# Kernel tuning notes

Measured on AMD Instinct MI355X. Metric: run time of the kernel, lower is better.

## Reference

```python
import jax, jax.numpy as jnp
import numpy as np

N, TI, ENC_DIM, DEC_DIM, ATT_DIM = 32, 2000, 512, 512, 512


def setup_inputs() -> dict:
    key = jax.random.key(0)
    ks = jax.random.split(key, 8)
    enc_pad = jax.random.normal(ks[0], (N, TI, ENC_DIM), dtype=jnp.float32)
    dec_prev = jax.random.normal(ks[1], (N, DEC_DIM), dtype=jnp.float32)
    ali_prev = jax.random.uniform(ks[2], (N, TI), dtype=jnp.float32)
    # lengths in [Ti//2, Ti], force one full-length row (module uses max(enc_len) as mask width)
    enc_len = jax.random.randint(ks[3], (N,), TI // 2, TI + 1)
    enc_len = enc_len.at[0].set(TI)
    # learned params (nn.Linear layout: W [out, in])
    s_e = 1.0 / np.sqrt(ENC_DIM)
    s_d = 1.0 / np.sqrt(DEC_DIM)
    s_a = 1.0 / np.sqrt(ATT_DIM)
    W_enc = jax.random.uniform(ks[4], (ATT_DIM, ENC_DIM), minval=-s_e, maxval=s_e, dtype=jnp.float32)
    b_enc = jax.random.uniform(ks[5], (ATT_DIM,), minval=-s_e, maxval=s_e, dtype=jnp.float32)
    W_dec = jax.random.uniform(ks[6], (ATT_DIM, DEC_DIM), minval=-s_d, maxval=s_d, dtype=jnp.float32)
    w_v = jax.random.uniform(ks[7], (ATT_DIM,), minval=-s_a, maxval=s_a, dtype=jnp.float32)
    return {"enc_pad": enc_pad, "enc_len": enc_len, "dec_prev": dec_prev,
            "ali_prev": ali_prev, "W_enc": W_enc, "b_enc": b_enc,
            "W_dec": W_dec, "w_v": w_v}


def reference(enc_pad, enc_len, dec_prev, ali_prev, W_enc, b_enc, W_dec, w_v):
    # enc_part: N x Ti x A  (enc_proj with bias)
    enc_part = jnp.einsum('ntd,ad->nta', enc_pad, W_enc) + b_enc
    # dec_part: N x A  (dec_proj, no bias)
    dec_part = jnp.einsum('nd,ad->na', dec_prev, W_dec)
    # additive score e = w^T tanh(enc_part + dec_part): N x Ti
    e = jnp.einsum('nta,a->nt', jnp.tanh(enc_part + dec_part[:, None, :]), w_v)
    # padding mask: positions >= enc_len are masked
    mask = jnp.arange(e.shape[1]) >= enc_len[:, None]  # N x Ti
    e = jnp.where(mask, -jnp.inf, e)
    ali = jax.nn.softmax(e, axis=1)  # N x Ti
    ctx = jnp.einsum('nt,ntd->nd', ali, enc_pad)  # N x D_enc
    return (ali, ctx)
```

## Files before the change

kernel.cpp:

```cpp
#include <hip/hip_runtime.h>
#include <stdint.h>


#define NB  32
#define TI  2000
#define ED  512
#define AD  512
#define M_TOT (NB * TI)
#define NSPLIT 20
#define TCHUNK (TI / NSPLIT)
#define MTS 500
#define NKS 16

using f16x8 = __attribute__((ext_vector_type(8))) _Float16;
using f32x4 = __attribute__((ext_vector_type(4))) float;

#define GLD16(g, l)                                                     \
    __builtin_amdgcn_global_load_lds(                                   \
        (const __attribute__((address_space(1))) void*)(g),             \
        (__attribute__((address_space(3))) void*)(l), 16, 0, 0)

__device__ __forceinline__ float fast_tanh(float s) {
    s = fminf(fmaxf(s, -15.f), 15.f);
    float t = __expf(2.f * s);
    return __fdividef(t - 1.f, t + 1.f);
}

__device__ __forceinline__ f16x8 cvt8(float4 a, float4 b) {
    f16x8 h;
    h[0] = (_Float16)a.x; h[1] = (_Float16)a.y; h[2] = (_Float16)a.z; h[3] = (_Float16)a.w;
    h[4] = (_Float16)b.x; h[5] = (_Float16)b.y; h[6] = (_Float16)b.z; h[7] = (_Float16)b.w;
    return h;
}

__global__ void k_wconvert(const float* __restrict__ Wenc, _Float16* __restrict__ W16,
                           const float* __restrict__ dec_prev, const float* __restrict__ W_dec,
                           const float* __restrict__ b_enc, float* __restrict__ db) {
    __shared__ float xd[ED];
    int bx = blockIdx.x;
    int tid = threadIdx.x;
    if (bx >= 128) {
        int n = bx - 128;
        for (int k = tid; k < ED; k += 256) xd[k] = dec_prev[n * ED + k];
        __syncthreads();
        for (int a = tid; a < AD; a += 256) {
            const float* wr = W_dec + (size_t)a * ED;
            float s = 0.f;
#pragma unroll 8
            for (int k = 0; k < ED; k += 4) {
                float4 w = *(const float4*)(wr + k);
                s += xd[k] * w.x + xd[k + 1] * w.y + xd[k + 2] * w.z + xd[k + 3] * w.w;
            }
            db[n * AD + a] = s + b_enc[a];
        }
        return;
    }
    int idx = bx * 4096 + tid * 16;
    int ks  = idx >> 15;
    int r   = idx & 32767;
    int gk  = r >> 13;
    int a   = (r & 8191) >> 4;
    int k   = ks * 32 + gk * 8;
    const float* s = Wenc + (size_t)a * ED + k;
    float4 x0 = *(const float4*)s;
    float4 x1 = *(const float4*)(s + 4);
    *(f16x8*)((char*)W16 + idx) = cvt8(x0, x1);
}

__global__ void k_decdb(const float* __restrict__ dec_prev,
                        const float* __restrict__ W_dec,
                        const float* __restrict__ b_enc,
                        float* __restrict__ db) {
    int n = blockIdx.x;
    __shared__ float xd[ED];
    for (int k = threadIdx.x; k < ED; k += 256) xd[k] = dec_prev[n * ED + k];
    __syncthreads();
    for (int a = threadIdx.x; a < AD; a += 256) {
        const float* wr = W_dec + (size_t)a * ED;
        float s = 0.f;
#pragma unroll 8
        for (int k = 0; k < ED; k += 4) {
            float4 w = *(const float4*)(wr + k);
            s += xd[k] * w.x + xd[k + 1] * w.y + xd[k + 2] * w.z + xd[k + 3] * w.w;
        }
        db[n * AD + a] = s + b_enc[a];
    }
}

__launch_bounds__(1024, 1)
__global__ void k_score256(const float* __restrict__ enc, const _Float16* __restrict__ W16,
                           const float* __restrict__ db, const float* __restrict__ wv,
                           float* __restrict__ e_out) {
    __shared__ alignas(16) char As0[16384];
    __shared__ alignas(16) char As1[16384];
    __shared__ alignas(16) char Bs0[32768];
    __shared__ alignas(16) char Bs1[32768];

    const int mt   = blockIdx.x;
    const int tid  = threadIdx.x;
    const int lane = tid & 63;
    const int w    = tid >> 6;
    const int wm   = w >> 3;
    const int wn   = w & 7;
    const int m0   = mt * 128;
    const int lr   = lane & 15;
    const int gk   = lane >> 4;

    const int arow = tid >> 3;
    const int sq   = (tid & 7) * 16;
    const int sqx  = (sq ^ ((arow & 7) << 4)) >> 2;
    const float* asrc = enc + (size_t)(m0 + arow) * ED + sqx;

    const char* wbase = (const char*)W16;

    f32x4 acc[4][4];
#pragma unroll
    for (int rb = 0; rb < 4; ++rb)
#pragma unroll
        for (int cb = 0; cb < 4; ++cb) acc[rb][cb] = (f32x4){0.f, 0.f, 0.f, 0.f};

#define STAGE(ks, dA, dB)                                               \
    {                                                                   \
        GLD16(asrc + (ks) * 32, (dA) + tid * 16);                       \
        const char* wsl = wbase + ((ks) << 15);                         \
        GLD16(wsl + tid * 16,          (dB) + tid * 16);                \
        GLD16(wsl + 16384 + tid * 16,  (dB) + 16384 + tid * 16);        \
    }

#define COMPUTE(sA, sB)                                                          \
    {                                                                            \
        f16x8 aF[4], bF[4];                                                      \
        _Pragma("unroll")                                                        \
        for (int rb = 0; rb < 4; ++rb) {                                         \
            int row = wm * 64 + rb * 16 + lr;                                    \
            int b0  = row * 128 + gk * 32;                                       \
            int sw  = (row & 7) << 4;                                            \
            f32x4 lo = *(const f32x4*)((sA) + (b0 ^ sw));                        \
            f32x4 hi = *(const f32x4*)((sA) + ((b0 + 16) ^ sw));                 \
            f16x8 h;                                                             \
            h[0] = (_Float16)lo[0]; h[1] = (_Float16)lo[1];                      \
            h[2] = (_Float16)lo[2]; h[3] = (_Float16)lo[3];                      \
            h[4] = (_Float16)hi[0]; h[5] = (_Float16)hi[1];                      \
            h[6] = (_Float16)hi[2]; h[7] = (_Float16)hi[3];                      \
            aF[rb] = h;                                                          \
        }                                                                        \
        _Pragma("unroll")                                                        \
        for (int cb = 0; cb < 4; ++cb) {                                         \
            int brow = wn * 64 + cb * 16 + lr;                                   \
            bF[cb] = *(const f16x8*)((sB) + gk * 8192 + brow * 16);              \
        }                                                                        \
        __builtin_amdgcn_s_setprio(1);                                           \
        _Pragma("unroll")                                                        \
        for (int rb = 0; rb < 4; ++rb)                                           \
            _Pragma("unroll")                                                    \
            for (int cb = 0; cb < 4; ++cb)                                       \
                acc[rb][cb] = __builtin_amdgcn_mfma_f32_16x16x32_f16(            \
                    aF[rb], bF[cb], acc[rb][cb], 0, 0, 0);                       \
        __builtin_amdgcn_s_setprio(0);                                           \
    }

#define ITER(k, Ac, Bc, An, Bn)  STAGE(k + 1, An, Bn); COMPUTE(Ac, Bc); __syncthreads();

    STAGE(0, As0, Bs0); __syncthreads();
    ITER(0,  As0, Bs0, As1, Bs1)
    ITER(1,  As1, Bs1, As0, Bs0)
    ITER(2,  As0, Bs0, As1, Bs1)
    ITER(3,  As1, Bs1, As0, Bs0)
    ITER(4,  As0, Bs0, As1, Bs1)
    ITER(5,  As1, Bs1, As0, Bs0)
    ITER(6,  As0, Bs0, As1, Bs1)
    ITER(7,  As1, Bs1, As0, Bs0)
    ITER(8,  As0, Bs0, As1, Bs1)
    ITER(9,  As1, Bs1, As0, Bs0)
    ITER(10, As0, Bs0, As1, Bs1)
    ITER(11, As1, Bs1, As0, Bs0)
    ITER(12, As0, Bs0, As1, Bs1)
    ITER(13, As1, Bs1, As0, Bs0)
    ITER(14, As0, Bs0, As1, Bs1)
    COMPUTE(As1, Bs1); __syncthreads();
#undef ITER
#undef COMPUTE
#undef STAGE

    float* e_red = (float*)As0;
    float wvv[4];
#pragma unroll
    for (int cb = 0; cb < 4; ++cb) wvv[cb] = wv[wn * 64 + cb * 16 + lr];

#pragma unroll
    for (int rb = 0; rb < 4; ++rb) {
#pragma unroll
        for (int i = 0; i < 4; ++i) {
            int row_local = wm * 64 + rb * 16 + gk * 4 + i;
            int m = m0 + row_local;
            int n = m / TI;
            const float* dbp = db + (size_t)n * AD + wn * 64;
            float rs = 0.f;
#pragma unroll
            for (int cb = 0; cb < 4; ++cb) {
                float s = acc[rb][cb][i] + dbp[cb * 16 + lr];
                rs += fast_tanh(s) * wvv[cb];
            }
            rs += __shfl_xor(rs, 1);
            rs += __shfl_xor(rs, 2);
            rs += __shfl_xor(rs, 4);
            rs += __shfl_xor(rs, 8);
            if (lr == 0) e_red[wn * 128 + row_local] = rs;
        }
    }
    __syncthreads();
    if (tid < 128) {
        float s = 0.f;
#pragma unroll
        for (int q = 0; q < 8; ++q) s += e_red[q * 128 + tid];
        e_out[m0 + tid] = s;
    }
}

__launch_bounds__(256, 2)
__global__ void k_score_fb(const float* __restrict__ X, const float* __restrict__ W,
                           const float* __restrict__ db, const float* __restrict__ wv,
                           float* __restrict__ e_part) {
    __shared__ alignas(16) _Float16 Xs[128][72];
    __shared__ alignas(16) _Float16 Ws[128][72];
    __shared__ float e_red[2][128];

    const int tid = threadIdx.x, lane = tid & 63, wid = tid >> 6;
    const int wr = wid >> 1, wc = wid & 1;
    const int m0 = blockIdx.x * 128, a0 = blockIdx.y * 128;

    f32x4 acc[4][4];
#pragma unroll
    for (int rb = 0; rb < 4; ++rb)
#pragma unroll
        for (int cb = 0; cb < 4; ++cb) acc[rb][cb] = (f32x4){0.f, 0.f, 0.f, 0.f};

    const int lr = lane & 15;
    const int lk = (lane >> 4) << 3;

    for (int kt = 0; kt < ED; kt += 64) {
#pragma unroll
        for (int i = 0; i < 4; ++i) {
            int idx = tid + i * 256, r = idx >> 3, c = (idx & 7) << 3;
            const float* gx = X + (size_t)(m0 + r) * ED + kt + c;
            float4 x0 = *(const float4*)gx, x1 = *(const float4*)(gx + 4);
            *(f16x8*)&Xs[r][c] = cvt8(x0, x1);
            const float* gw = W + (size_t)(a0 + r) * ED + kt + c;
            float4 w0 = *(const float4*)gw, w1 = *(const float4*)(gw + 4);
            *(f16x8*)&Ws[r][c] = cvt8(w0, w1);
        }
        __syncthreads();
#pragma unroll
        for (int kb = 0; kb < 64; kb += 32) {
            f16x8 aF[4], bF[4];
#pragma unroll
            for (int rb = 0; rb < 4; ++rb) aF[rb] = *(const f16x8*)&Xs[wr * 64 + rb * 16 + lr][kb + lk];
#pragma unroll
            for (int cb = 0; cb < 4; ++cb) bF[cb] = *(const f16x8*)&Ws[wc * 64 + cb * 16 + lr][kb + lk];
#pragma unroll
            for (int rb = 0; rb < 4; ++rb)
#pragma unroll
                for (int cb = 0; cb < 4; ++cb)
                    acc[rb][cb] = __builtin_amdgcn_mfma_f32_16x16x32_f16(aF[rb], bF[cb], acc[rb][cb], 0, 0, 0);
        }
        __syncthreads();
    }

    const int lg = lane >> 4;
    float wvv[4];
#pragma unroll
    for (int cb = 0; cb < 4; ++cb) wvv[cb] = wv[a0 + wc * 64 + cb * 16 + lr];
#pragma unroll
    for (int rb = 0; rb < 4; ++rb) {
#pragma unroll
        for (int i = 0; i < 4; ++i) {
            int row_local = wr * 64 + rb * 16 + lg * 4 + i;
            int m = m0 + row_local;
            int n = m / TI;
            const float* dbp = db + (size_t)n * AD + a0 + wc * 64;
            float rs = 0.f;
#pragma unroll
            for (int cb = 0; cb < 4; ++cb) {
                float s = acc[rb][cb][i] + dbp[cb * 16 + lr];
                rs += fast_tanh(s) * wvv[cb];
            }
            rs += __shfl_xor(rs, 1);
            rs += __shfl_xor(rs, 2);
            rs += __shfl_xor(rs, 4);
            rs += __shfl_xor(rs, 8);
            if (lr == 0) e_red[wc][row_local] = rs;
        }
    }
    __syncthreads();
    if (tid < 128)
        e_part[(size_t)blockIdx.y * M_TOT + m0 + tid] = e_red[0][tid] + e_red[1][tid];
}

__global__ void k_softmax(const float* __restrict__ e_part,
                          const int* __restrict__ enc_len,
                          float* __restrict__ ali, int nparts) {
    int n = blockIdx.x;
    int len = enc_len[n];
    __shared__ float se[TI];
    __shared__ float redm[4];
    __shared__ float reds[4];
    int tid = threadIdx.x;
    int lane = tid & 63, wid = tid >> 6;

    for (int t = tid; t < TI; t += 256) {
        float s = 0.f;
        for (int p = 0; p < nparts; ++p) s += e_part[(size_t)p * M_TOT + n * TI + t];
        se[t] = s;
    }
    __syncthreads();

    float mx = -1e30f;
    for (int t = tid; t < len; t += 256) mx = fmaxf(mx, se[t]);
#pragma unroll
    for (int o = 32; o >= 1; o >>= 1) mx = fmaxf(mx, __shfl_xor(mx, o));
    if (lane == 0) redm[wid] = mx;
    __syncthreads();
    mx = fmaxf(fmaxf(redm[0], redm[1]), fmaxf(redm[2], redm[3]));

    float sm = 0.f;
    for (int t = tid; t < len; t += 256) {
        float ex = __expf(se[t] - mx);
        se[t] = ex;
        sm += ex;
    }
#pragma unroll
    for (int o = 32; o >= 1; o >>= 1) sm += __shfl_xor(sm, o);
    if (lane == 0) reds[wid] = sm;
    __syncthreads();
    float inv = 1.f / (reds[0] + reds[1] + reds[2] + reds[3]);

    for (int t = tid; t < TI; t += 256)
        ali[n * TI + t] = (t < len) ? se[t] * inv : 0.f;
}

__global__ void k_ctxpart(const float* __restrict__ enc,
                          const float* __restrict__ ali,
                          float* __restrict__ cpart) {
    int s = blockIdx.x;
    int n = blockIdx.y;
    int d0 = threadIdx.x * 2;
    const float* base = enc + ((size_t)n * TI + s * TCHUNK) * ED + d0;
    const float* ap = ali + n * TI + s * TCHUNK;
    float ax = 0.f, ay = 0.f;
#pragma unroll 4
    for (int t = 0; t < TCHUNK; ++t) {
        float a = ap[t];
        float2 v = *(const float2*)(base + (size_t)t * ED);
        ax = fmaf(a, v.x, ax);
        ay = fmaf(a, v.y, ay);
    }
    float2 r; r.x = ax; r.y = ay;
    *(float2*)&cpart[((size_t)(n * NSPLIT + s)) * ED + d0] = r;
}

__global__ void k_ctxred(const float* __restrict__ cpart, float* __restrict__ ctx) {
    int n = blockIdx.x;
    for (int d = threadIdx.x; d < ED; d += 256) {
        float sum = 0.f;
#pragma unroll
        for (int s = 0; s < NSPLIT; ++s) sum += cpart[((size_t)(n * NSPLIT + s)) * ED + d];
        ctx[(size_t)n * ED + d] = sum;
    }
}

extern "C" void kernel_launch(void* const* d_in, const int* in_sizes, int n_in,
                              void* d_out, int out_size, void* d_ws, size_t ws_size,
                              hipStream_t stream) {
    const float* enc_pad  = (const float*)d_in[0];
    const int*   enc_len  = (const int*)d_in[1];
    const float* dec_prev = (const float*)d_in[2];
    const float* W_enc    = (const float*)d_in[4];
    const float* b_enc    = (const float*)d_in[5];
    const float* W_dec    = (const float*)d_in[6];
    const float* w_v      = (const float*)d_in[7];

    float* out = (float*)d_out;
    float* ali = out;
    float* ctx = out + M_TOT;

    float* ws     = (float*)d_ws;
    float* db     = ws;
    float* e_part = ws + NB * AD;
    float* cpart  = e_part + 4 * M_TOT;
    size_t fp_floats = (size_t)NB * AD + 4 * M_TOT + (size_t)NB * NSPLIT * ED;
    _Float16* W16 = (_Float16*)((char*)d_ws + fp_floats * 4);
    size_t need = fp_floats * 4 + (size_t)512 * 1024;
    bool big = ws_size >= need;

    if (big) {
        hipLaunchKernelGGL(k_wconvert, dim3(160), dim3(256), 0, stream,
                           W_enc, W16, dec_prev, W_dec, b_enc, db);
        hipLaunchKernelGGL(k_score256, dim3(MTS), dim3(1024), 0, stream,
                           enc_pad, W16, db, w_v, e_part);
        hipLaunchKernelGGL(k_softmax, dim3(NB), dim3(256), 0, stream, e_part, enc_len, ali, 1);
    } else {
        hipLaunchKernelGGL(k_decdb, dim3(NB), dim3(256), 0, stream, dec_prev, W_dec, b_enc, db);
        hipLaunchKernelGGL(k_score_fb, dim3(M_TOT / 128, 4), dim3(256), 0, stream,
                           enc_pad, W_enc, db, w_v, e_part);
        hipLaunchKernelGGL(k_softmax, dim3(NB), dim3(256), 0, stream, e_part, enc_len, ali, 4);
    }
    hipLaunchKernelGGL(k_ctxpart, dim3(NSPLIT, NB), dim3(256), 0, stream, enc_pad, ali, cpart);
    hipLaunchKernelGGL(k_ctxred, dim3(NB), dim3(256), 0, stream, cpart, ctx);
}
```

Measured before the change: 122.0 us.

## Restructure score GEMM to 64-row tiles with 512 threads and bulk A staging

The score kernel now uses 64-row M tiles with 8 waves of 512 threads, launching 1000 blocks instead of 500. Each block loads its whole fp32 enc tile into LDS in two 64KB halves and streams only the fp16 W slices per K step through a single B buffer. Synchronisation now uses explicit vmcnt waits and raw barriers. The aim is more blocks in flight and fewer per-step global A loads, at the cost of about 160KB of LDS per block, a single-buffered B that serialises loading with compute, and reading the W matrix twice as often in total.

Result: slower. 165.4 us (+35.6%).

```diff
diff --git a/kernel.cpp b/kernel.cpp
--- a/kernel.cpp
+++ b/kernel.cpp
@@ -9,7 +9,7 @@
 #define M_TOT (NB * TI)
 #define NSPLIT 20
 #define TCHUNK (TI / NSPLIT)
-#define MTS 500
+#define MTS 1000
 #define NKS 16
 
 using f16x8 = __attribute__((ext_vector_type(8))) _Float16;
@@ -87,29 +87,25 @@
     }
 }
 
-__launch_bounds__(1024, 1)
+__launch_bounds__(512, 1)
 __global__ void k_score256(const float* __restrict__ enc, const _Float16* __restrict__ W16,
                            const float* __restrict__ db, const float* __restrict__ wv,
                            float* __restrict__ e_out) {
-    __shared__ alignas(16) char As0[16384];
-    __shared__ alignas(16) char As1[16384];
-    __shared__ alignas(16) char Bs0[32768];
-    __shared__ alignas(16) char Bs1[32768];
+    __shared__ alignas(16) char As0[65536];
+    __shared__ alignas(16) char As1[65536];
+    __shared__ alignas(16) char Bs[32768];
 
     const int mt   = blockIdx.x;
     const int tid  = threadIdx.x;
     const int lane = tid & 63;
     const int w    = tid >> 6;
-    const int wm   = w >> 3;
-    const int wn   = w & 7;
-    const int m0   = mt * 128;
+    const int wn   = w;
+    const int m0   = mt * 64;
     const int lr   = lane & 15;
     const int gk   = lane >> 4;
 
-    const int arow = tid >> 3;
-    const int sq   = (tid & 7) * 16;
-    const int sqx  = (sq ^ ((arow & 7) << 4)) >> 2;
-    const float* asrc = enc + (size_t)(m0 + arow) * ED + sqx;
+    const int arow_base = tid >> 6;
+    const int awithin   = (tid & 63) * 16;
 
     const char* wbase = (const char*)W16;
 
@@ -119,21 +115,30 @@
 #pragma unroll
         for (int cb = 0; cb < 4; ++cb) acc[rb][cb] = (f32x4){0.f, 0.f, 0.f, 0.f};
 
-#define STAGE(ks, dA, dB)                                               \
+#define STAGE_A(c, half, dst)                                              \
+    {                                                                      \
+        int row_ = (c) * 8 + arow_base;                                    \
+        int g_   = (awithin ^ ((row_ & 7) << 4)) >> 2;                     \
+        const float* gp_ = enc + (size_t)(m0 + row_) * ED + (half) * 256 + g_; \
+        GLD16(gp_, (dst) + (c) * 8192 + tid * 16);                         \
+    }
+
+#define STAGE_B(ks)                                                     \
     {                                                                   \
-        GLD16(asrc + (ks) * 32, (dA) + tid * 16);                       \
         const char* wsl = wbase + ((ks) << 15);                         \
-        GLD16(wsl + tid * 16,          (dB) + tid * 16);                \
-        GLD16(wsl + 16384 + tid * 16,  (dB) + 16384 + tid * 16);        \
-    }
-
-#define COMPUTE(sA, sB)                                                          \
+        GLD16(wsl + tid * 16,          Bs + tid * 16);                  \
+        GLD16(wsl + 8192 + tid * 16,   Bs + 8192 + tid * 16);           \
+        GLD16(wsl + 16384 + tid * 16,  Bs + 16384 + tid * 16);          \
+        GLD16(wsl + 24576 + tid * 16,  Bs + 24576 + tid * 16);          \
+    }
+
+#define COMPUTE(ksl, sA)                                                         \
     {                                                                            \
         f16x8 aF[4], bF[4];                                                      \
         _Pragma("unroll")                                                        \
         for (int rb = 0; rb < 4; ++rb) {                                         \
-            int row = wm * 64 + rb * 16 + lr;                                    \
-            int b0  = row * 128 + gk * 32;                                       \
+            int row = rb * 16 + lr;                                              \
+            int b0  = row * 1024 + (ksl) * 128 + gk * 32;                        \
             int sw  = (row & 7) << 4;                                            \
             f32x4 lo = *(const f32x4*)((sA) + (b0 ^ sw));                        \
             f32x4 hi = *(const f32x4*)((sA) + ((b0 + 16) ^ sw));                 \
@@ -147,7 +152,7 @@
         _Pragma("unroll")                                                        \
         for (int cb = 0; cb < 4; ++cb) {                                         \
             int brow = wn * 64 + cb * 16 + lr;                                   \
-            bF[cb] = *(const f16x8*)((sB) + gk * 8192 + brow * 16);              \
+            bF[cb] = *(const f16x8*)(Bs + gk * 8192 + brow * 16);                \
         }                                                                        \
         __builtin_amdgcn_s_setprio(1);                                           \
         _Pragma("unroll")                                                        \
@@ -159,28 +164,43 @@
         __builtin_amdgcn_s_setprio(0);                                           \
     }
 
-#define ITER(k, Ac, Bc, An, Bn)  STAGE(k + 1, An, Bn); COMPUTE(Ac, Bc); __syncthreads();
-
-    STAGE(0, As0, Bs0); __syncthreads();
-    ITER(0,  As0, Bs0, As1, Bs1)
-    ITER(1,  As1, Bs1, As0, Bs0)
-    ITER(2,  As0, Bs0, As1, Bs1)
-    ITER(3,  As1, Bs1, As0, Bs0)
-    ITER(4,  As0, Bs0, As1, Bs1)
-    ITER(5,  As1, Bs1, As0, Bs0)
-    ITER(6,  As0, Bs0, As1, Bs1)
-    ITER(7,  As1, Bs1, As0, Bs0)
-    ITER(8,  As0, Bs0, As1, Bs1)
-    ITER(9,  As1, Bs1, As0, Bs0)
-    ITER(10, As0, Bs0, As1, Bs1)
-    ITER(11, As1, Bs1, As0, Bs0)
-    ITER(12, As0, Bs0, As1, Bs1)
-    ITER(13, As1, Bs1, As0, Bs0)
-    ITER(14, As0, Bs0, As1, Bs1)
-    COMPUTE(As1, Bs1); __syncthreads();
-#undef ITER
+#define WAITV0 { asm volatile("s_waitcnt vmcnt(0)" ::: "memory"); __builtin_amdgcn_sched_barrier(0); }
+#define WAITV1 { asm volatile("s_waitcnt vmcnt(1)" ::: "memory"); __builtin_amdgcn_sched_barrier(0); }
+#define BAR __builtin_amdgcn_s_barrier()
+
+#pragma unroll
+    for (int c = 0; c < 8; ++c) STAGE_A(c, 0, As0);
+    STAGE_B(0);
+    WAITV0; BAR;
+
+#pragma unroll
+    for (int k = 0; k < 7; ++k) {
+        COMPUTE(k, As0);
+        BAR;
+        STAGE_B(k + 1);
+        STAGE_A(k, 1, As1);
+        WAITV1; BAR;
+    }
+    COMPUTE(7, As0);
+    BAR;
+    STAGE_B(8);
+    STAGE_A(7, 1, As1);
+    WAITV0; BAR;
+#pragma unroll
+    for (int k = 8; k < 15; ++k) {
+        COMPUTE(k - 8, As1);
+        BAR;
+        STAGE_B(k + 1);
+        WAITV0; BAR;
+    }
+    COMPUTE(7, As1);
+    __syncthreads();
+#undef WAITV0
+#undef WAITV1
+#undef BAR
 #undef COMPUTE
-#undef STAGE
+#undef STAGE_B
+#undef STAGE_A
 
     float* e_red = (float*)As0;
     float wvv[4];
@@ -191,7 +211,7 @@
     for (int rb = 0; rb < 4; ++rb) {
 #pragma unroll
         for (int i = 0; i < 4; ++i) {
-            int row_local = wm * 64 + rb * 16 + gk * 4 + i;
+            int row_local = rb * 16 + gk * 4 + i;
             int m = m0 + row_local;
             int n = m / TI;
             const float* dbp = db + (size_t)n * AD + wn * 64;
@@ -205,14 +225,14 @@
             rs += __shfl_xor(rs, 2);
             rs += __shfl_xor(rs, 4);
             rs += __shfl_xor(rs, 8);
-            if (lr == 0) e_red[wn * 128 + row_local] = rs;
-        }
-    }
-    __syncthreads();
-    if (tid < 128) {
+            if (lr == 0) e_red[wn * 64 + row_local] = rs;
+        }
+    }
+    __syncthreads();
+    if (tid < 64) {
         float s = 0.f;
 #pragma unroll
-        for (int q = 0; q < 8; ++q) s += e_red[q * 128 + tid];
+        for (int q = 0; q < 8; ++q) s += e_red[q * 64 + tid];
         e_out[m0 + tid] = s;
     }
 }
@@ -395,7 +415,7 @@
     if (big) {
         hipLaunchKernelGGL(k_wconvert, dim3(160), dim3(256), 0, stream,
                            W_enc, W16, dec_prev, W_dec, b_enc, db);
-        hipLaunchKernelGGL(k_score256, dim3(MTS), dim3(1024), 0, stream,
+        hipLaunchKernelGGL(k_score256, dim3(MTS), dim3(512), 0, stream,
                            enc_pad, W16, db, w_v, e_part);
         hipLaunchKernelGGL(k_softmax, dim3(NB), dim3(256), 0, stream, e_part, enc_len, ali, 1);
     } else {
```

## Split score GEMM into two 256-column tiles with 512-thread blocks

Applied to the files above, without the earlier changes.

The fused score kernel now gives each block 128 rows and half of the attention columns (256) using 512 threads, instead of all 512 columns with 1024 threads. Two blocks can share a CU, and a grouped block-index mapping keeps the pair of column halves for the same rows adjacent so the enc tile is likely reused from cache. The two column halves write separate partial scores, which the softmax kernel then sums (two partials). The trade-off is that enc rows are loaded twice from global memory, and fp16 conversion of A is repeated per half.

New measurement: 132.5 us (median of 3 runs). 1.09x slower.

```diff
diff --git a/kernel.cpp b/kernel.cpp
--- a/kernel.cpp
+++ b/kernel.cpp
@@ -87,31 +87,41 @@
     }
 }
 
-__launch_bounds__(1024, 1)
+__launch_bounds__(512, 2)
 __global__ void k_score256(const float* __restrict__ enc, const _Float16* __restrict__ W16,
                            const float* __restrict__ db, const float* __restrict__ wv,
-                           float* __restrict__ e_out) {
+                           float* __restrict__ e_part) {
     __shared__ alignas(16) char As0[16384];
     __shared__ alignas(16) char As1[16384];
-    __shared__ alignas(16) char Bs0[32768];
-    __shared__ alignas(16) char Bs1[32768];
-
-    const int mt   = blockIdx.x;
+    __shared__ alignas(16) char Bs0[16384];
+    __shared__ alignas(16) char Bs1[16384];
+
+    int fid = blockIdx.x;
+    int g = fid >> 4, r = fid & 15;
+    int at2 = r >> 3;
+    int mt  = g * 8 + (r & 7);
+    if (mt >= MTS) return;
+
     const int tid  = threadIdx.x;
     const int lane = tid & 63;
     const int w    = tid >> 6;
-    const int wm   = w >> 3;
-    const int wn   = w & 7;
+    const int wm   = w >> 2;
+    const int wn   = w & 3;
     const int m0   = mt * 128;
+    const int a0   = at2 * 256;
     const int lr   = lane & 15;
     const int gk   = lane >> 4;
 
-    const int arow = tid >> 3;
-    const int sq   = (tid & 7) * 16;
-    const int sqx  = (sq ^ ((arow & 7) << 4)) >> 2;
-    const float* asrc = enc + (size_t)(m0 + arow) * ED + sqx;
+    const int da   = tid * 16;
+    const int arow = da >> 7;
+    const int aswz = ((da & 127) ^ ((arow & 7) << 4)) >> 2;
+    const float* asrc = enc + (size_t)(m0 + arow) * ED + aswz;
 
     const char* wbase = (const char*)W16;
+    const int db0 = tid * 16;
+    const int db1 = db0 + 8192;
+    const int bs0 = ((db0 >> 12) << 13) + at2 * 4096 + (db0 & 4095);
+    const int bs1 = ((db1 >> 12) << 13) + at2 * 4096 + (db1 & 4095);
 
     f32x4 acc[4][4];
 #pragma unroll
@@ -121,10 +131,11 @@
 
 #define STAGE(ks, dA, dB)                                               \
     {                                                                   \
-        GLD16(asrc + (ks) * 32, (dA) + tid * 16);                       \
+        GLD16(asrc + (ks) * 32,            (dA) + da);                  \
+        GLD16(asrc + 64 * ED + (ks) * 32,  (dA) + da + 8192);           \
         const char* wsl = wbase + ((ks) << 15);                         \
-        GLD16(wsl + tid * 16,          (dB) + tid * 16);                \
-        GLD16(wsl + 16384 + tid * 16,  (dB) + 16384 + tid * 16);        \
+        GLD16(wsl + bs0, (dB) + db0);                                   \
+        GLD16(wsl + bs1, (dB) + db1);                                   \
     }
 
 #define COMPUTE(sA, sB)                                                          \
@@ -147,7 +158,7 @@
         _Pragma("unroll")                                                        \
         for (int cb = 0; cb < 4; ++cb) {                                         \
             int brow = wn * 64 + cb * 16 + lr;                                   \
-            bF[cb] = *(const f16x8*)((sB) + gk * 8192 + brow * 16);              \
+            bF[cb] = *(const f16x8*)((sB) + gk * 4096 + brow * 16);              \
         }                                                                        \
         __builtin_amdgcn_s_setprio(1);                                           \
         _Pragma("unroll")                                                        \
@@ -185,7 +196,7 @@
     float* e_red = (float*)As0;
     float wvv[4];
 #pragma unroll
-    for (int cb = 0; cb < 4; ++cb) wvv[cb] = wv[wn * 64 + cb * 16 + lr];
+    for (int cb = 0; cb < 4; ++cb) wvv[cb] = wv[a0 + wn * 64 + cb * 16 + lr];
 
 #pragma unroll
     for (int rb = 0; rb < 4; ++rb) {
@@ -194,7 +205,7 @@
             int row_local = wm * 64 + rb * 16 + gk * 4 + i;
             int m = m0 + row_local;
             int n = m / TI;
-            const float* dbp = db + (size_t)n * AD + wn * 64;
+            const float* dbp = db + (size_t)n * AD + a0 + wn * 64;
             float rs = 0.f;
 #pragma unroll
             for (int cb = 0; cb < 4; ++cb) {
@@ -209,12 +220,9 @@
         }
     }
     __syncthreads();
-    if (tid < 128) {
-        float s = 0.f;
-#pragma unroll
-        for (int q = 0; q < 8; ++q) s += e_red[q * 128 + tid];
-        e_out[m0 + tid] = s;
-    }
+    if (tid < 128)
+        e_part[(size_t)at2 * M_TOT + m0 + tid] =
+            e_red[tid] + e_red[128 + tid] + e_red[256 + tid] + e_red[384 + tid];
 }
 
 __launch_bounds__(256, 2)
@@ -395,9 +403,9 @@
     if (big) {
         hipLaunchKernelGGL(k_wconvert, dim3(160), dim3(256), 0, stream,
                            W_enc, W16, dec_prev, W_dec, b_enc, db);
-        hipLaunchKernelGGL(k_score256, dim3(MTS), dim3(1024), 0, stream,
+        hipLaunchKernelGGL(k_score256, dim3(1008), dim3(512), 0, stream,
                            enc_pad, W16, db, w_v, e_part);
-        hipLaunchKernelGGL(k_softmax, dim3(NB), dim3(256), 0, stream, e_part, enc_len, ali, 1);
+        hipLaunchKernelGGL(k_softmax, dim3(NB), dim3(256), 0, stream, e_part, enc_len, ali, 2);
     } else {
         hipLaunchKernelGGL(k_decdb, dim3(NB), dim3(256), 0, stream, dec_prev, W_dec, b_enc, db);
         hipLaunchKernelGGL(k_score_fb, dim3(M_TOT / 128, 4), dim3(256), 0, stream,
```
